# Kernel tuning notes

Measured on AMD Instinct MI355X. Metric: run time of the kernel, lower is better.

Reference implementation:

```python
import jax, jax.numpy as jnp
import numpy as np

N = 30000      # num_nodes
R0 = 8         # original relations
R = 2 * R0 + 1 # with inverses + self-loop relation = 17
IN = 256
OUT = 256
E = 300000     # original triples
NB = 8         # num_bases


def setup_inputs() -> dict:
    key = jax.random.key(0)
    k1, k2, k3, k4, k5, k6 = jax.random.split(key, 6)
    s = jax.random.randint(k1, (E,), 0, N)
    r = jax.random.randint(k2, (E,), 0, R0)
    o = jax.random.randint(k3, (E,), 0, N)
    triples = jnp.stack([s, r, o], axis=1)  # [E,3] int
    features = jax.random.normal(k4, (N, IN), dtype=jnp.float32)
    bases = jax.random.normal(k5, (NB, IN, OUT), dtype=jnp.float32) * 0.02
    comps = jax.random.normal(k6, (R, NB), dtype=jnp.float32) * 0.02
    bias = jnp.zeros((OUT,), dtype=jnp.float32)
    return {"triples": triples, "features": features, "bases": bases, "comps": comps, "bias": bias}


def reference(triples, features, bases, comps, bias):
    # basis decomposition: weights[r] = sum_b comps[r,b] * bases[b]
    weights = jnp.einsum('rb,bio->rio', comps, bases)  # [R, IN, OUT]

    s, r, o = triples[:, 0], triples[:, 1], triples[:, 2]
    nodes = jnp.arange(N)
    # eval mode: self_loop_keep_prob = 1 -> all N self loops kept
    src = jnp.concatenate([s, o, nodes])                                  # [E + E + N]
    rel = jnp.concatenate([r, r + R0, jnp.full((N,), 2 * R0, r.dtype)])
    dst = jnp.concatenate([o, s, nodes])

    # horizontal stacking: adj is [N, R*N]; row = src, col = rel*N + dst
    cols = rel * N + dst
    # column normalisation (row_normalisation=False branch of sum_sparse)
    col_sums = jnp.zeros((R * N,), jnp.float32).at[cols].add(1.0)
    sums = col_sums[cols]
    # reorder: swap normalizers of original and inverse edge blocks
    sums = jnp.concatenate([sums[E:2 * E], sums[:E], sums[2 * E:]])
    vals = 1.0 / sums

    # fw[r*N + n] = features[n] @ weights[r]
    fw = jnp.einsum('ni,rio->rno', features, weights).reshape(R * N, OUT)
    msgs = vals[:, None] * fw[cols]                    # [num_edges, OUT]
    out = jnp.zeros((N, OUT), jnp.float32).at[src].add(msgs)
    return out + bias
```

## Files before the change

kernel.cpp:

```cpp
#include <hip/hip_runtime.h>


namespace {
constexpr int kN     = 30000;
constexpr int kR0    = 8;
constexpr int kNRel  = 16;
constexpr int kIN    = 256;
constexpr int kOUT   = 256;
constexpr int kE     = 300000;
constexpr int kNB    = 8;
constexpr int kKT    = kNB * kIN;
constexpr int kRows  = kN * kNRel;
constexpr int kMsgs  = 2 * kE;
constexpr int kScanBlk  = 1024;
constexpr int kNScanBlk = (kRows + kScanBlk - 1) / kScanBlk;
constexpr int kBM    = 64;
constexpr int kMB    = (kN + kBM - 1) / kBM;
constexpr int kMPad  = kMB * kBM;
constexpr int kTN    = 16;
}

typedef __bf16 bf16x8 __attribute__((ext_vector_type(8)));
typedef float  f32x4  __attribute__((ext_vector_type(4)));
typedef unsigned int u32;

static __device__ __forceinline__ ushort f2bf(float x) {
  unsigned u = __float_as_uint(x);
  u += 0x7FFF + ((u >> 16) & 1);
  return (ushort)(u >> 16);
}

static __device__ __forceinline__ void gload16(const void* g, void* l) {
  __builtin_amdgcn_global_load_lds(
      (const __attribute__((address_space(1))) u32*)g,
      (__attribute__((address_space(3))) u32*)l, 16, 0, 0);
}


__global__ void k_fbf(const float* __restrict__ f, ushort* __restrict__ fb) {
  int i = blockIdx.x * 256 + threadIdx.x;
  if (i >= kN * kIN / 4) return;
  float4 v = reinterpret_cast<const float4*>(f)[i];
  ushort4 p;
  p.x = f2bf(v.x); p.y = f2bf(v.y); p.z = f2bf(v.z); p.w = f2bf(v.w);
  reinterpret_cast<ushort4*>(fb)[i] = p;
}

__global__ void k_bt(const float* __restrict__ bases, ushort* __restrict__ Bt) {
  __shared__ float tile[16][256];
  int b = blockIdx.x;
  int t = threadIdx.x;
#pragma unroll
  for (int kk = 0; kk < 16; ++kk)
    tile[kk][t] = bases[(size_t)(b * 16 + kk) * kOUT + t];
  __syncthreads();
  char* dst = (char*)Bt + (size_t)t * 4096;
  int xr = (t & 7) << 4;
#pragma unroll
  for (int q = 0; q < 4; ++q) {
    ushort4 p;
    p.x = f2bf(tile[q*4+0][t]); p.y = f2bf(tile[q*4+1][t]);
    p.z = f2bf(tile[q*4+2][t]); p.w = f2bf(tile[q*4+3][t]);
    *reinterpret_cast<ushort4*>(dst + ((b * 32 + q * 8) ^ xr)) = p;
  }
}


__global__ void k_count(const int* __restrict__ t, int* __restrict__ deg) {
  int e = blockIdx.x * 256 + threadIdx.x;
  if (e >= kE) return;
  int s = t[3*e], r = t[3*e+1], o = t[3*e+2];
  atomicAdd(&deg[s * kNRel + r], 1);
  atomicAdd(&deg[o * kNRel + kR0 + r], 1);
}

__global__ void k_scan1(const int* __restrict__ deg, int* __restrict__ rp,
                        int* __restrict__ blksum) {
  __shared__ int s[256];
  int tid = threadIdx.x;
  int base = blockIdx.x * kScanBlk + tid * 4;
  int v0 = 0, v1 = 0, v2 = 0, v3 = 0;
  if (base + 3 < kRows) {
    v0 = deg[base]; v1 = deg[base+1]; v2 = deg[base+2]; v3 = deg[base+3];
  } else {
    if (base     < kRows) v0 = deg[base];
    if (base + 1 < kRows) v1 = deg[base+1];
    if (base + 2 < kRows) v2 = deg[base+2];
  }
  int t0 = v0, t1 = t0 + v1, t2 = t1 + v2, t3 = t2 + v3;
  s[tid] = t3;
  __syncthreads();
  for (int off = 1; off < 256; off <<= 1) {
    int x = 0;
    if (tid >= off) x = s[tid - off];
    __syncthreads();
    s[tid] += x;
    __syncthreads();
  }
  int excl = tid ? s[tid-1] : 0;
  if (base     < kRows) rp[base]   = excl;
  if (base + 1 < kRows) rp[base+1] = excl + t0;
  if (base + 2 < kRows) rp[base+2] = excl + t1;
  if (base + 3 < kRows) rp[base+3] = excl + t2;
  if (tid == 255) blksum[blockIdx.x] = s[255];
}

__global__ void k_scan2(int* __restrict__ blksum) {
  __shared__ int s[512];
  int tid = threadIdx.x;
  s[tid] = (tid < kNScanBlk) ? blksum[tid] : 0;
  __syncthreads();
  for (int off = 1; off < 512; off <<= 1) {
    int x = 0;
    if (tid >= off) x = s[tid - off];
    __syncthreads();
    s[tid] += x;
    __syncthreads();
  }
  if (tid < kNScanBlk) blksum[tid] = tid ? s[tid-1] : 0;
}

__global__ void k_scan3(int* __restrict__ rp, const int* __restrict__ blksum) {
  int i = blockIdx.x * 256 + threadIdx.x;
  if (i < kRows)       rp[i] += blksum[i >> 10];
  else if (i == kRows) rp[i]  = kMsgs;
}

__global__ void k_scatter(const int* __restrict__ t, const int* __restrict__ rp,
                          int* __restrict__ cursor, int* __restrict__ col) {
  int m = blockIdx.x * 256 + threadIdx.x;
  if (m >= kMsgs) return;
  int e = (m < kE) ? m : m - kE;
  int s = t[3*e], r = t[3*e+1], o = t[3*e+2];
  int rr, tn, sn;
  if (m < kE) { rr = r;        tn = s; sn = o; }
  else        { rr = kR0 + r;  tn = o; sn = s; }
  int idx = tn * kNRel + rr;
  int pos = rp[idx] + atomicAdd(&cursor[idx], 1);
  col[pos] = (rr << 16) | sn;
}

#define FMA4(A, S, G) \
  A.x += (S) * G.x; A.y += (S) * G.y; A.z += (S) * G.z; A.w += (S) * G.w;


__global__ __launch_bounds__(256, 6)
void k_agg1(const int* __restrict__ rp, const int* __restrict__ col,
            const float* __restrict__ feat, const ushort* __restrict__ featbf,
            const float* __restrict__ comps, ushort* __restrict__ aggb) {
  __shared__ float cvb[4][17][kNB];
  int wv   = threadIdx.x >> 6;
  int lane = threadIdx.x & 63;
  int node = blockIdx.x * 4 + wv;

  if (lane < 17) {
    float val = 0.f;
    if (lane < kNRel) {
      int idx = node * kNRel + lane;
      int d = rp[idx + 1] - rp[idx];
      val = d > 0 ? 1.0f / (float)d : 0.f;
    }
#pragma unroll
    for (int b = 0; b < kNB; ++b)
      cvb[wv][lane][b] = comps[lane * kNB + b] * val;
  }
  __syncthreads();

  int e0 = rp[node * kNRel];
  int e1 = rp[node * kNRel + kNRel];

  float4 f = *reinterpret_cast<const float4*>(feat + (size_t)node * kIN + lane * 4);
  float4 acc[kNB];
#pragma unroll
  for (int b = 0; b < kNB; ++b) {
    float cs = comps[2*kR0*kNB + b];
    acc[b].x = cs * f.x; acc[b].y = cs * f.y; acc[b].z = cs * f.z; acc[b].w = cs * f.w;
  }

  const float4* cvr = reinterpret_cast<const float4*>(&cvb[wv][0][0]);
  const int pad = (16 << 16);
  int cc[4];
#pragma unroll
  for (int j = 0; j < 4; ++j) {
    int ee = e0 + j;
    int v  = col[ee < kMsgs ? ee : kMsgs - 1];
    cc[j] = ee < e1 ? v : pad;
  }
  for (int e = e0; e < e1; e += 4) {
    uint2 g[4];
#pragma unroll
    for (int j = 0; j < 4; ++j) {
      int sn = cc[j] & 0xFFFF;
      g[j] = *reinterpret_cast<const uint2*>(featbf + (size_t)sn * kIN + lane * 4);
    }
    int rr[4];
#pragma unroll
    for (int j = 0; j < 4; ++j) rr[j] = cc[j] >> 16;
#pragma unroll
    for (int j = 0; j < 4; ++j) {
      int ee = e + 4 + j;
      int v  = col[ee < kMsgs ? ee : kMsgs - 1];
      cc[j] = ee < e1 ? v : pad;
    }
#pragma unroll
    for (int j = 0; j < 4; ++j) {
      float4 c0 = cvr[rr[j] * 2];
      float4 c1 = cvr[rr[j] * 2 + 1];
      float4 gg;
      gg.x = __uint_as_float(g[j].x << 16);
      gg.y = __uint_as_float(g[j].x & 0xFFFF0000u);
      gg.z = __uint_as_float(g[j].y << 16);
      gg.w = __uint_as_float(g[j].y & 0xFFFF0000u);
      FMA4(acc[0], c0.x, gg) FMA4(acc[1], c0.y, gg)
      FMA4(acc[2], c0.z, gg) FMA4(acc[3], c0.w, gg)
      FMA4(acc[4], c1.x, gg) FMA4(acc[5], c1.y, gg)
      FMA4(acc[6], c1.z, gg) FMA4(acc[7], c1.w, gg)
    }
  }

  char* rowp = (char*)aggb + (size_t)node * 4096;
  int xr = (node & 7) << 4;
#pragma unroll
  for (int b = 0; b < kNB; ++b) {
    ushort4 p;
    p.x = f2bf(acc[b].x); p.y = f2bf(acc[b].y);
    p.z = f2bf(acc[b].z); p.w = f2bf(acc[b].w);
    *reinterpret_cast<ushort4*>(rowp + ((b * 512 + lane * 8) ^ xr)) = p;
  }
}


__global__ __launch_bounds__(512, 4)
void k_gemm(const ushort* __restrict__ aggb, const ushort* __restrict__ Bt,
            const float* __restrict__ bias, float* __restrict__ out) {
  __shared__ ushort Albs[kBM * 128];
  __shared__ ushort Blds[256 * 128];
  int tid  = threadIdx.x;
  int wv   = tid >> 6;
  int lane = tid & 63;
  int mh   = wv >> 2;
  int nq   = wv & 3;
  int l15  = lane & 15;
  int g4   = lane >> 4;
  int node0 = blockIdx.x * kBM;

  f32x4 acc[2][4];
#pragma unroll
  for (int mt = 0; mt < 2; ++mt)
#pragma unroll
    for (int nt = 0; nt < 4; ++nt) acc[mt][nt] = f32x4{0.f, 0.f, 0.f, 0.f};

  for (int c = 0; c < 16; ++c) {
#pragma unroll
    for (int i = 0; i < 2; ++i) {
      int seg = i * 8 + wv;
      int lin = seg * 1024 + lane * 16;
      int row = lin >> 8;
      const char* src = (const char*)aggb + (size_t)(node0 + row) * 4096
                        + c * 256 + (lin & 255);
      gload16(src, (char*)Albs + seg * 1024);
    }
#pragma unroll
    for (int i = 0; i < 8; ++i) {
      int seg = i * 8 + wv;
      int lin = seg * 1024 + lane * 16;
      int colr = lin >> 8;
      const char* src = (const char*)Bt + (size_t)colr * 4096
                        + c * 256 + (lin & 255);
      gload16(src, (char*)Blds + seg * 1024);
    }
    asm volatile("s_waitcnt vmcnt(0)" ::: "memory");
    __syncthreads();

#pragma unroll
    for (int ks = 0; ks < 4; ++ks) {
      int kb = ks * 64 + g4 * 16;
      bf16x8 a[2], b[4];
#pragma unroll
      for (int mt = 0; mt < 2; ++mt) {
        int row = mh * 32 + mt * 16 + l15;
        a[mt] = *reinterpret_cast<const bf16x8*>(
            (const char*)Albs + row * 256 + (kb ^ ((row & 7) << 4)));
      }
#pragma unroll
      for (int nt = 0; nt < 4; ++nt) {
        int colr = nq * 64 + nt * 16 + l15;
        b[nt] = *reinterpret_cast<const bf16x8*>(
            (const char*)Blds + colr * 256 + (kb ^ ((colr & 7) << 4)));
      }
#pragma unroll
      for (int mt = 0; mt < 2; ++mt)
#pragma unroll
        for (int nt = 0; nt < 4; ++nt)
          acc[mt][nt] = __builtin_amdgcn_mfma_f32_16x16x32_bf16(a[mt], b[nt],
                                                                acc[mt][nt], 0, 0, 0);
    }
    __syncthreads();
  }

#pragma unroll
  for (int nt = 0; nt < 4; ++nt) {
    int colo = nq * 64 + nt * 16 + l15;
    float bi = bias[colo];
#pragma unroll
    for (int mt = 0; mt < 2; ++mt) {
      int rbase = node0 + mh * 32 + mt * 16 + g4 * 4;
#pragma unroll
      for (int j = 0; j < 4; ++j) {
        int row = rbase + j;
        if (row < kN) out[(size_t)row * kOUT + colo] = acc[mt][nt][j] + bi;
      }
    }
  }
}


__global__ __launch_bounds__(512, 4)
void k_out_fused(const int* __restrict__ rp, const int* __restrict__ col,
                 const float* __restrict__ feat, const ushort* __restrict__ featbf,
                 const ushort* __restrict__ Bt, const float* __restrict__ comps,
                 const float* __restrict__ bias, float* __restrict__ out) {
  __shared__ ushort aggs[kTN * kKT];
  __shared__ float  cvb[kTN][17][kNB];
  int tid  = threadIdx.x;
  int wv   = tid >> 6;
  int lane = tid & 63;
  int node0 = blockIdx.x * kTN;

  for (int q = tid; q < kTN * 17; q += 512) {
    int nl = q / 17, rl = q - nl * 17;
    float val = 0.f;
    if (rl < kNRel) {
      int idx = (node0 + nl) * kNRel + rl;
      int d = rp[idx + 1] - rp[idx];
      val = d > 0 ? 1.0f / (float)d : 0.f;
    }
#pragma unroll
    for (int b = 0; b < kNB; ++b)
      cvb[nl][rl][b] = comps[rl * kNB + b] * val;
  }
  __syncthreads();

  for (int half = 0; half < 2; ++half) {
    int nl   = (wv << 1) | half;
    int node = node0 + nl;
    int e0 = rp[node * kNRel];
    int e1 = rp[node * kNRel + kNRel];

    float4 f = *reinterpret_cast<const float4*>(feat + (size_t)node * kIN + lane * 4);
    float4 acc[kNB];
#pragma unroll
    for (int b = 0; b < kNB; ++b) {
      float cs = comps[2*kR0*kNB + b];
      acc[b].x = cs * f.x; acc[b].y = cs * f.y; acc[b].z = cs * f.z; acc[b].w = cs * f.w;
    }
    const float4* cvr = reinterpret_cast<const float4*>(&cvb[nl][0][0]);
    const int pad = (16 << 16);
    int cc[4];
#pragma unroll
    for (int j = 0; j < 4; ++j) {
      int ee = e0 + j;
      int v  = col[ee < kMsgs ? ee : kMsgs - 1];
      cc[j] = ee < e1 ? v : pad;
    }
    for (int e = e0; e < e1; e += 4) {
      uint2 g[4];
#pragma unroll
      for (int j = 0; j < 4; ++j) {
        int sn = cc[j] & 0xFFFF;
        g[j] = *reinterpret_cast<const uint2*>(featbf + (size_t)sn * kIN + lane * 4);
      }
      int rr[4];
#pragma unroll
      for (int j = 0; j < 4; ++j) rr[j] = cc[j] >> 16;
#pragma unroll
      for (int j = 0; j < 4; ++j) {
        int ee = e + 4 + j;
        int v  = col[ee < kMsgs ? ee : kMsgs - 1];
        cc[j] = ee < e1 ? v : pad;
      }
#pragma unroll
      for (int j = 0; j < 4; ++j) {
        float4 c0 = cvr[rr[j] * 2];
        float4 c1 = cvr[rr[j] * 2 + 1];
        float4 gg;
        gg.x = __uint_as_float(g[j].x << 16);
        gg.y = __uint_as_float(g[j].x & 0xFFFF0000u);
        gg.z = __uint_as_float(g[j].y << 16);
        gg.w = __uint_as_float(g[j].y & 0xFFFF0000u);
        FMA4(acc[0], c0.x, gg) FMA4(acc[1], c0.y, gg)
        FMA4(acc[2], c0.z, gg) FMA4(acc[3], c0.w, gg)
        FMA4(acc[4], c1.x, gg) FMA4(acc[5], c1.y, gg)
        FMA4(acc[6], c1.z, gg) FMA4(acc[7], c1.w, gg)
      }
    }
    int xr = (nl & 7) << 4;
#pragma unroll
    for (int b = 0; b < kNB; ++b) {
      ushort4 p;
      p.x = f2bf(acc[b].x); p.y = f2bf(acc[b].y);
      p.z = f2bf(acc[b].z); p.w = f2bf(acc[b].w);
      int byteoff = nl * 4096 + ((b * 512 + lane * 8) ^ xr);
      *reinterpret_cast<ushort4*>(reinterpret_cast<char*>(aggs) + byteoff) = p;
    }
  }
  __syncthreads();

  {
    int n  = lane & 15;
    int g4 = lane >> 4;
    const char* abase = reinterpret_cast<const char*>(aggs) + n * 4096;
    int axor = (n & 7) << 4;
#pragma unroll
    for (int t = 0; t < 2; ++t) {
      int ntile = wv + t * 8;
      float bi = bias[ntile * 16 + n];
      const char* btrow = reinterpret_cast<const char*>(Bt)
                          + (size_t)(ntile * 16 + n) * 4096;
      int bxor = (n & 7) << 4;
      f32x4 acc = {0.f, 0.f, 0.f, 0.f};
#pragma unroll 4
      for (int ks = 0; ks < kKT / 32; ++ks) {
        int kb = ks * 64 + g4 * 16;
        bf16x8 af = *reinterpret_cast<const bf16x8*>(abase + (kb ^ axor));
        bf16x8 bf = *reinterpret_cast<const bf16x8*>(btrow + (kb ^ bxor));
        acc = __builtin_amdgcn_mfma_f32_16x16x32_bf16(af, bf, acc, 0, 0, 0);
      }
#pragma unroll
      for (int j = 0; j < 4; ++j) {
        int row = g4 * 4 + j;
        out[(size_t)(node0 + row) * kOUT + ntile * 16 + n] = acc[j] + bi;
      }
    }
  }
}


extern "C" void kernel_launch(void* const* d_in, const int* in_sizes, int n_in,
                              void* d_out, int out_size, void* d_ws, size_t ws_size,
                              hipStream_t stream) {
  const int*   triples = (const int*)  d_in[0];
  const float* feat    = (const float*)d_in[1];
  const float* bases   = (const float*)d_in[2];
  const float* comps   = (const float*)d_in[3];
  const float* bias    = (const float*)d_in[4];
  float* out = (float*)d_out;

  size_t featbf_b = (size_t)kN * kIN * 2;
  size_t bt_b     = (size_t)kOUT * kKT * 2;
  size_t aggb_b   = (size_t)kMPad * kKT * 2;
  size_t csr_b    = (size_t)(kRows + kRows + 1 + kMsgs + kNScanBlk) * 4;
  bool bigws = ws_size >= featbf_b + bt_b + aggb_b + csr_b + 1024;

  char* p = (char*)d_ws;
  ushort* featbf = (ushort*)p;            p += featbf_b;
  ushort* Bt     = (ushort*)p;            p += bt_b;
  ushort* aggb   = nullptr;
  if (bigws) { aggb = (ushort*)p;         p += aggb_b; }
  int* deg    = (int*)p;
  int* rp     = deg + kRows;
  int* col    = rp + kRows + 1;
  int* blksum = col + kMsgs;

  k_fbf   <<<(kN * kIN / 4 + 255) / 256, 256, 0, stream>>>(feat, featbf);
  k_bt    <<<kKT / 16,            256, 0, stream>>>(bases, Bt);
  hipMemsetAsync(deg, 0, kRows * sizeof(int), stream);
  k_count <<<(kE + 255) / 256,    256, 0, stream>>>(triples, deg);
  k_scan1 <<<kNScanBlk,           256, 0, stream>>>(deg, rp, blksum);
  k_scan2 <<<1,                   512, 0, stream>>>(blksum);
  k_scan3 <<<(kRows + 256) / 256, 256, 0, stream>>>(rp, blksum);
  hipMemsetAsync(deg, 0, kRows * sizeof(int), stream);
  k_scatter<<<(kMsgs + 255) / 256, 256, 0, stream>>>(triples, rp, deg, col);

  if (bigws) {
    k_agg1<<<kN / 4,  256, 0, stream>>>(rp, col, feat, featbf, comps, aggb);
    k_gemm<<<kMB,     512, 0, stream>>>(aggb, Bt, bias, out);
  } else {
    k_out_fused<<<kN / kTN, 512, 0, stream>>>(rp, col, feat, featbf, Bt,
                                              comps, bias, out);
  }
}
```

Before: 192.0 us.

## Fuse prep kernels, drop memset, software-pipeline gather and double-buffer GEMM

Merges the bf16 feature conversion and the degree counting into one kernel. The scatter now counts degrees down instead of up, which removes the second memset. The aggregation loop prefetches the next group's gathered features one iteration ahead (occupancy hint lowered from 6 to 4 to make room for the extra registers). The GEMM now stages half-width K chunks into double-buffered LDS so the next chunk's loads overlap the current MFMAs. Together these aim to cut launch count, memory latency stalls and GEMM load/compute serialisation, at the cost of higher register pressure and lower occupancy.

```diff
diff --git a/kernel.cpp b/kernel.cpp
--- a/kernel.cpp
+++ b/kernel.cpp
@@ -37,13 +37,20 @@
 }
 
 
-__global__ void k_fbf(const float* __restrict__ f, ushort* __restrict__ fb) {
+__global__ void k_prep(const float* __restrict__ f, ushort* __restrict__ fb,
+                       const int* __restrict__ t, int* __restrict__ deg) {
   int i = blockIdx.x * 256 + threadIdx.x;
-  if (i >= kN * kIN / 4) return;
-  float4 v = reinterpret_cast<const float4*>(f)[i];
-  ushort4 p;
-  p.x = f2bf(v.x); p.y = f2bf(v.y); p.z = f2bf(v.z); p.w = f2bf(v.w);
-  reinterpret_cast<ushort4*>(fb)[i] = p;
+  if (i < kN * kIN / 4) {
+    float4 v = reinterpret_cast<const float4*>(f)[i];
+    ushort4 p;
+    p.x = f2bf(v.x); p.y = f2bf(v.y); p.z = f2bf(v.z); p.w = f2bf(v.w);
+    reinterpret_cast<ushort4*>(fb)[i] = p;
+  }
+  if (i < kE) {
+    int s = t[3*i], r = t[3*i+1], o = t[3*i+2];
+    atomicAdd(&deg[s * kNRel + r], 1);
+    atomicAdd(&deg[o * kNRel + kR0 + r], 1);
+  }
 }
 
 __global__ void k_bt(const float* __restrict__ bases, ushort* __restrict__ Bt) {
@@ -65,14 +72,6 @@
   }
 }
 
-
-__global__ void k_count(const int* __restrict__ t, int* __restrict__ deg) {
-  int e = blockIdx.x * 256 + threadIdx.x;
-  if (e >= kE) return;
-  int s = t[3*e], r = t[3*e+1], o = t[3*e+2];
-  atomicAdd(&deg[s * kNRel + r], 1);
-  atomicAdd(&deg[o * kNRel + kR0 + r], 1);
-}
 
 __global__ void k_scan1(const int* __restrict__ deg, int* __restrict__ rp,
                         int* __restrict__ blksum) {
@@ -127,7 +126,7 @@
 }
 
 __global__ void k_scatter(const int* __restrict__ t, const int* __restrict__ rp,
-                          int* __restrict__ cursor, int* __restrict__ col) {
+                          int* __restrict__ deg, int* __restrict__ col) {
   int m = blockIdx.x * 256 + threadIdx.x;
   if (m >= kMsgs) return;
   int e = (m < kE) ? m : m - kE;
@@ -136,7 +135,7 @@
   if (m < kE) { rr = r;        tn = s; sn = o; }
   else        { rr = kR0 + r;  tn = o; sn = s; }
   int idx = tn * kNRel + rr;
-  int pos = rp[idx] + atomicAdd(&cursor[idx], 1);
+  int pos = rp[idx] + (atomicSub(&deg[idx], 1) - 1);
   col[pos] = (rr << 16) | sn;
 }
 
@@ -144,7 +143,7 @@
   A.x += (S) * G.x; A.y += (S) * G.y; A.z += (S) * G.z; A.w += (S) * G.w;
 
 
-__global__ __launch_bounds__(256, 6)
+__global__ __launch_bounds__(256, 4)
 void k_agg1(const int* __restrict__ rp, const int* __restrict__ col,
             const float* __restrict__ feat, const ushort* __restrict__ featbf,
             const float* __restrict__ comps, ushort* __restrict__ aggb) {
@@ -179,42 +178,56 @@
 
   const float4* cvr = reinterpret_cast<const float4*>(&cvb[wv][0][0]);
   const int pad = (16 << 16);
-  int cc[4];
+
+  int cc0[4], cc1[4];
+  uint2 g0[4];
 #pragma unroll
   for (int j = 0; j < 4; ++j) {
     int ee = e0 + j;
     int v  = col[ee < kMsgs ? ee : kMsgs - 1];
-    cc[j] = ee < e1 ? v : pad;
-  }
+    cc0[j] = ee < e1 ? v : pad;
+  }
+#pragma unroll
+  for (int j = 0; j < 4; ++j)
+    g0[j] = *reinterpret_cast<const uint2*>(featbf + (size_t)(cc0[j] & 0xFFFF) * kIN + lane * 4);
+#pragma unroll
+  for (int j = 0; j < 4; ++j) {
+    int ee = e0 + 4 + j;
+    int v  = col[ee < kMsgs ? ee : kMsgs - 1];
+    cc1[j] = ee < e1 ? v : pad;
+  }
+
+#pragma unroll 2
   for (int e = e0; e < e1; e += 4) {
-    uint2 g[4];
+    uint2 g1[4];
+#pragma unroll
+    for (int j = 0; j < 4; ++j)
+      g1[j] = *reinterpret_cast<const uint2*>(featbf + (size_t)(cc1[j] & 0xFFFF) * kIN + lane * 4);
+    int cc2[4];
 #pragma unroll
     for (int j = 0; j < 4; ++j) {
-      int sn = cc[j] & 0xFFFF;
-      g[j] = *reinterpret_cast<const uint2*>(featbf + (size_t)sn * kIN + lane * 4);
-    }
-    int rr[4];
-#pragma unroll
-    for (int j = 0; j < 4; ++j) rr[j] = cc[j] >> 16;
+      int ee = e + 8 + j;
+      int v  = col[ee < kMsgs ? ee : kMsgs - 1];
+      cc2[j] = ee < e1 ? v : pad;
+    }
 #pragma unroll
     for (int j = 0; j < 4; ++j) {
-      int ee = e + 4 + j;
-      int v  = col[ee < kMsgs ? ee : kMsgs - 1];
-      cc[j] = ee < e1 ? v : pad;
-    }
-#pragma unroll
-    for (int j = 0; j < 4; ++j) {
-      float4 c0 = cvr[rr[j] * 2];
-      float4 c1 = cvr[rr[j] * 2 + 1];
+      int r = cc0[j] >> 16;
+      float4 c0 = cvr[r * 2];
+      float4 c1 = cvr[r * 2 + 1];
       float4 gg;
-      gg.x = __uint_as_float(g[j].x << 16);
-      gg.y = __uint_as_float(g[j].x & 0xFFFF0000u);
-      gg.z = __uint_as_float(g[j].y << 16);
-      gg.w = __uint_as_float(g[j].y & 0xFFFF0000u);
+      gg.x = __uint_as_float(g0[j].x << 16);
+      gg.y = __uint_as_float(g0[j].x & 0xFFFF0000u);
+      gg.z = __uint_as_float(g0[j].y << 16);
+      gg.w = __uint_as_float(g0[j].y & 0xFFFF0000u);
       FMA4(acc[0], c0.x, gg) FMA4(acc[1], c0.y, gg)
       FMA4(acc[2], c0.z, gg) FMA4(acc[3], c0.w, gg)
       FMA4(acc[4], c1.x, gg) FMA4(acc[5], c1.y, gg)
       FMA4(acc[6], c1.z, gg) FMA4(acc[7], c1.w, gg)
+    }
+#pragma unroll
+    for (int j = 0; j < 4; ++j) {
+      cc0[j] = cc1[j]; cc1[j] = cc2[j]; g0[j] = g1[j];
     }
   }
 
@@ -233,8 +246,8 @@
 __global__ __launch_bounds__(512, 4)
 void k_gemm(const ushort* __restrict__ aggb, const ushort* __restrict__ Bt,
             const float* __restrict__ bias, float* __restrict__ out) {
-  __shared__ ushort Albs[kBM * 128];
-  __shared__ ushort Blds[256 * 128];
+  __shared__ ushort Albs[2][kBM * 64];
+  __shared__ ushort Blds[2][256 * 64];
   int tid  = threadIdx.x;
   int wv   = tid >> 6;
   int lane = tid & 63;
@@ -250,43 +263,47 @@
 #pragma unroll
     for (int nt = 0; nt < 4; ++nt) acc[mt][nt] = f32x4{0.f, 0.f, 0.f, 0.f};
 
-  for (int c = 0; c < 16; ++c) {
-#pragma unroll
-    for (int i = 0; i < 2; ++i) {
-      int seg = i * 8 + wv;
+  auto stage = [&](int c, int buf) {
+    {
+      int lin = wv * 1024 + lane * 16;
+      int row = lin >> 7;
+      const char* src = (const char*)aggb + (size_t)(node0 + row) * 4096
+                        + c * 128 + (lin & 127);
+      gload16(src, (char*)Albs[buf] + wv * 1024);
+    }
+#pragma unroll
+    for (int i = 0; i < 4; ++i) {
+      int seg = wv * 4 + i;
       int lin = seg * 1024 + lane * 16;
-      int row = lin >> 8;
-      const char* src = (const char*)aggb + (size_t)(node0 + row) * 4096
-                        + c * 256 + (lin & 255);
-      gload16(src, (char*)Albs + seg * 1024);
-    }
-#pragma unroll
-    for (int i = 0; i < 8; ++i) {
-      int seg = i * 8 + wv;
-      int lin = seg * 1024 + lane * 16;
-      int colr = lin >> 8;
+      int colr = lin >> 7;
       const char* src = (const char*)Bt + (size_t)colr * 4096
-                        + c * 256 + (lin & 255);
-      gload16(src, (char*)Blds + seg * 1024);
-    }
-    asm volatile("s_waitcnt vmcnt(0)" ::: "memory");
-    __syncthreads();
-
-#pragma unroll
-    for (int ks = 0; ks < 4; ++ks) {
+                        + c * 128 + (lin & 127);
+      gload16(src, (char*)Blds[buf] + seg * 1024);
+    }
+  };
+
+  stage(0, 0);
+  asm volatile("s_waitcnt vmcnt(0)" ::: "memory");
+  __syncthreads();
+
+  int cur = 0;
+  for (int c = 0; c < 32; ++c) {
+    if (c + 1 < 32) stage(c + 1, cur ^ 1);
+#pragma unroll
+    for (int ks = 0; ks < 2; ++ks) {
       int kb = ks * 64 + g4 * 16;
       bf16x8 a[2], b[4];
 #pragma unroll
       for (int mt = 0; mt < 2; ++mt) {
         int row = mh * 32 + mt * 16 + l15;
         a[mt] = *reinterpret_cast<const bf16x8*>(
-            (const char*)Albs + row * 256 + (kb ^ ((row & 7) << 4)));
+            (const char*)Albs[cur] + row * 128 + (kb ^ ((row & 7) << 4)));
       }
 #pragma unroll
       for (int nt = 0; nt < 4; ++nt) {
         int colr = nq * 64 + nt * 16 + l15;
         b[nt] = *reinterpret_cast<const bf16x8*>(
-            (const char*)Blds + colr * 256 + (kb ^ ((colr & 7) << 4)));
+            (const char*)Blds[cur] + colr * 128 + (kb ^ ((colr & 7) << 4)));
       }
 #pragma unroll
       for (int mt = 0; mt < 2; ++mt)
@@ -295,7 +312,9 @@
           acc[mt][nt] = __builtin_amdgcn_mfma_f32_16x16x32_bf16(a[mt], b[nt],
                                                                 acc[mt][nt], 0, 0, 0);
     }
+    asm volatile("s_waitcnt vmcnt(0)" ::: "memory");
     __syncthreads();
+    cur ^= 1;
   }
 
 #pragma unroll
@@ -462,14 +481,12 @@
   int* col    = rp + kRows + 1;
   int* blksum = col + kMsgs;
 
-  k_fbf   <<<(kN * kIN / 4 + 255) / 256, 256, 0, stream>>>(feat, featbf);
+  hipMemsetAsync(deg, 0, kRows * sizeof(int), stream);
+  k_prep  <<<(kN * kIN / 4 + 255) / 256, 256, 0, stream>>>(feat, featbf, triples, deg);
   k_bt    <<<kKT / 16,            256, 0, stream>>>(bases, Bt);
-  hipMemsetAsync(deg, 0, kRows * sizeof(int), stream);
-  k_count <<<(kE + 255) / 256,    256, 0, stream>>>(triples, deg);
   k_scan1 <<<kNScanBlk,           256, 0, stream>>>(deg, rp, blksum);
   k_scan2 <<<1,                   512, 0, stream>>>(blksum);
   k_scan3 <<<(kRows + 256) / 256, 256, 0, stream>>>(rp, blksum);
-  hipMemsetAsync(deg, 0, kRows * sizeof(int), stream);
   k_scatter<<<(kMsgs + 255) / 256, 256, 0, stream>>>(triples, rp, deg, col);
 
   if (bigws) {
```

New measurement: 190.7 us. About the same (-0.7%).
